# Performance work log

Hardware: AMD Instinct MI355X
Metric: run time of the kernel (lower is better)

Reference implementation:

```python
import jax, jax.numpy as jnp
import numpy as np

N, F, H, C = 4096, 512, 8, 128
LEAKY_ALPHA = 0.2
MASK_VAL = -10e9  # spektral uses -10e9 * (1 - A)


def setup_inputs() -> dict:
    key = jax.random.key(0)
    k1, k2, k3, k4, k5 = jax.random.split(key, 5)
    X = jax.random.normal(k1, (N, F), dtype=jnp.float32)
    # sparse-ish binary adjacency with self loops (dense layout as the layer expects)
    A = (jax.random.uniform(k2, (N, N)) < 0.01).astype(jnp.float32)
    A = jnp.maximum(A, jnp.eye(N, dtype=jnp.float32))
    W = jax.random.normal(k3, (H, F, C), dtype=jnp.float32) * (1.0 / np.sqrt(F))
    a_self = jax.random.normal(k4, (H, C), dtype=jnp.float32) * (1.0 / np.sqrt(C))
    a_neigh = jax.random.normal(k5, (H, C), dtype=jnp.float32) * (1.0 / np.sqrt(C))
    bias = jnp.zeros((H, C), dtype=jnp.float32)
    return {"X": X, "A": A, "W": W, "a_self": a_self, "a_neigh": a_neigh, "bias": bias}


def reference(X, A, W, a_self, a_neigh, bias):
    # per-head feature projection: [H, N, C]
    feats = jnp.einsum("nf,hfc->hnc", X, W)
    # attention scores e_ij = LeakyReLU(a_self . h_i + a_neigh . h_j)
    s_self = jnp.einsum("hnc,hc->hn", feats, a_self)    # [H, N]
    s_neigh = jnp.einsum("hnc,hc->hn", feats, a_neigh)  # [H, N]
    dense = s_self[:, :, None] + s_neigh[:, None, :]    # [H, N, N]
    dense = jnp.where(dense > 0, dense, LEAKY_ALPHA * dense)
    # adjacency mask then row softmax (dropout_rate=0 -> identity)
    dense = dense + MASK_VAL * (1.0 - A)[None, :, :]
    coef = jax.nn.softmax(dense, axis=-1)               # [H, N, N]
    out = jnp.einsum("hnm,hmc->hnc", coef, feats)       # [H, N, C]
    out = out + bias[:, None, :]
    # concat heads: [N, H*C]
    out = jnp.transpose(out, (1, 0, 2)).reshape(N, H * C)
    return jax.nn.relu(out)
```

## Files before the change

### kernel.cpp

```cpp
#include <hip/hip_runtime.h>
#include <hip/hip_bf16.h>

#define GN 4096
#define GF 512
#define GH 8
#define GC 128
#define CAP 256
#define XS 72

typedef __hip_bfloat16 bf16;
typedef unsigned short u16;
typedef unsigned int u32;
typedef __attribute__((ext_vector_type(8))) short bf16x8;
typedef __attribute__((ext_vector_type(4))) float f32x4;

static __device__ inline u16 f2u16(float x) {
    union { bf16 b; u16 u; } cv;
    cv.b = __float2bfloat16(x);
    return cv.u;
}

__global__ __launch_bounds__(256) void prep_csr_kernel(
    const float* __restrict__ A, const float* __restrict__ X,
    const float* __restrict__ W, int* __restrict__ deg,
    u16* __restrict__ lists, u16* __restrict__ Xb, u16* __restrict__ WT)
{
    __shared__ u16 sT[16][520];
    int tid = threadIdx.x;
    int b   = blockIdx.x;

    if (b < 1024) {
        size_t idx = ((size_t)b * 256 + tid) * 8;
        float4 v0 = *(const float4*)(X + idx);
        float4 v1 = *(const float4*)(X + idx + 4);
        u16 o[8] = {f2u16(v0.x), f2u16(v0.y), f2u16(v0.z), f2u16(v0.w),
                    f2u16(v1.x), f2u16(v1.y), f2u16(v1.z), f2u16(v1.w)};
        *(bf16x8*)(Xb + idx) = *(bf16x8*)o;
        return;
    }
    if (b < 1088) {
        int wb = b - 1024;
        int h  = wb >> 3;
        int s16 = (wb & 7) * 16;
        const float* Wh = W + (size_t)h * GF * GC;
        for (int pass = 0; pass < 8; ++pass) {
            int k  = pass * 64 + (tid >> 2);
            int n4 = tid & 3;
            float4 v = *(const float4*)&Wh[(size_t)k * GC + s16 + n4 * 4];
            sT[n4 * 4 + 0][k] = f2u16(v.x);
            sT[n4 * 4 + 1][k] = f2u16(v.y);
            sT[n4 * 4 + 2][k] = f2u16(v.z);
            sT[n4 * 4 + 3][k] = f2u16(v.w);
        }
        __syncthreads();
        int n = tid >> 4, seg = tid & 15;
        u16* dst = WT + ((size_t)h * GC + s16 + n) * GF + seg * 32;
#pragma unroll
        for (int s = 0; s < 4; ++s)
            *(bf16x8*)(dst + s * 8) = *(const bf16x8*)&sT[n][seg * 32 + s * 8];
        return;
    }

    int i    = b - 1088;
    int lane = tid & 63;
    int* cnt = (int*)&sT[0][0];
    if (tid == 0) *cnt = 0;
    __syncthreads();

    u16* row = lists + (size_t)i * CAP;
    const float4* Arow = (const float4*)(A + (size_t)i * GN);
    unsigned long long ltmask = (lane == 63) ? ~0ull >> 1
                                             : (1ull << lane) - 1;
#pragma unroll
    for (int it = 0; it < 4; ++it) {
        int qd = it * 256 + tid;
        float4 a = Arow[qd];
        int j = qd * 4;
#pragma unroll
        for (int comp = 0; comp < 4; ++comp) {
            float av = comp == 0 ? a.x : comp == 1 ? a.y : comp == 2 ? a.z : a.w;
            bool flag = av > 0.5f;
            unsigned long long m = __ballot(flag);
            if (m) {
                int base = 0;
                if (lane == 0) base = atomicAdd(cnt, __popcll(m));
                base = __shfl(base, 0);
                if (flag) {
                    int s = base + __popcll(m & ltmask);
                    if (s < CAP) row[s] = (u16)(j + comp);
                }
            }
        }
    }
    __syncthreads();
    if (tid == 0) deg[i] = *cnt < CAP ? *cnt : CAP;
}

__global__ __launch_bounds__(256) void feats_kernel(
    const u16* __restrict__ Xb, const u16* __restrict__ WT,
    const float* __restrict__ a_self, const float* __restrict__ a_neigh,
    bf16* __restrict__ featsb, float* __restrict__ s_self,
    float* __restrict__ s_neigh)
{
    __shared__ u16 sX[64 * XS];
    __shared__ u16 sW[128 * XS];

    int h   = blockIdx.x >> 6;
    int n0  = (blockIdx.x & 63) << 6;
    int tid = threadIdx.x;
    int lane = tid & 63, wv = tid >> 6;
    int lm = lane & 15, q = lane >> 4;

    const u16* Xp = Xb + (size_t)n0 * GF;
    const u16* Wp = WT + (size_t)h * GC * GF;

    uint4 xr[2], wr[4];

#define ISSUE_TILE(K0)                                                        \
    {                                                                         \
        _Pragma("unroll")                                                     \
        for (int it = 0; it < 2; ++it) {                                      \
            int idx = it * 256 + tid, row = idx >> 3, c = idx & 7;            \
            xr[it] = *(const uint4*)&Xp[(size_t)row * GF + (K0) + c * 8];     \
        }                                                                     \
        _Pragma("unroll")                                                     \
        for (int it = 0; it < 4; ++it) {                                      \
            int idx = it * 256 + tid, row = idx >> 3, c = idx & 7;            \
            wr[it] = *(const uint4*)&Wp[(size_t)row * GF + (K0) + c * 8];     \
        }                                                                     \
    }

#define STORE_TILE()                                                          \
    {                                                                         \
        _Pragma("unroll")                                                     \
        for (int it = 0; it < 2; ++it) {                                      \
            int idx = it * 256 + tid, row = idx >> 3, c = idx & 7;            \
            *(uint4*)&sX[row * XS + c * 8] = xr[it];                          \
        }                                                                     \
        _Pragma("unroll")                                                     \
        for (int it = 0; it < 4; ++it) {                                      \
            int idx = it * 256 + tid, row = idx >> 3, c = idx & 7;            \
            *(uint4*)&sW[row * XS + c * 8] = wr[it];                          \
        }                                                                     \
    }

    f32x4 acc[8];
#pragma unroll
    for (int nt = 0; nt < 8; ++nt) acc[nt] = (f32x4){0.f, 0.f, 0.f, 0.f};

    ISSUE_TILE(0)
    STORE_TILE()

    for (int k0 = 0; k0 < GF; k0 += 64) {
        __syncthreads();
        if (k0 + 64 < GF) ISSUE_TILE(k0 + 64)

#pragma unroll
        for (int ks = 0; ks < 64; ks += 32) {
            bf16x8 af = *(const bf16x8*)&sX[(wv * 16 + lm) * XS + ks + q * 8];
            bf16x8 bfr[8];
#pragma unroll
            for (int nt = 0; nt < 8; ++nt)
                bfr[nt] = *(const bf16x8*)&sW[(nt * 16 + lm) * XS + ks + q * 8];
#pragma unroll
            for (int nt = 0; nt < 8; ++nt)
                acc[nt] = __builtin_amdgcn_mfma_f32_16x16x32_bf16(
                    af, bfr[nt], acc[nt], 0, 0, 0);
        }
        __syncthreads();
        if (k0 + 64 < GF) STORE_TILE()
    }
#undef ISSUE_TILE
#undef STORE_TILE

    float aS[8], aN[8];
#pragma unroll
    for (int nt = 0; nt < 8; ++nt) {
        aS[nt] = a_self[h * GC + nt * 16 + lm];
        aN[nt] = a_neigh[h * GC + nt * 16 + lm];
    }
    float vs[4] = {0.f, 0.f, 0.f, 0.f};
    float vn[4] = {0.f, 0.f, 0.f, 0.f};
    int rbase = n0 + wv * 16 + q * 4;
#pragma unroll
    for (int nt = 0; nt < 8; ++nt) {
        f32x4 v = acc[nt];
        int col = nt * 16 + lm;
#pragma unroll
        for (int r = 0; r < 4; ++r) {
            featsb[((size_t)h * GN + rbase + r) * GC + col] = __float2bfloat16(v[r]);
            vs[r] += v[r] * aS[nt];
            vn[r] += v[r] * aN[nt];
        }
    }
#pragma unroll
    for (int r = 0; r < 4; ++r) {
        for (int off = 1; off < 16; off <<= 1) {
            vs[r] += __shfl_xor(vs[r], off);
            vn[r] += __shfl_xor(vn[r], off);
        }
        if (lm == 0) {
            s_self[h * GN + rbase + r]  = vs[r];
            s_neigh[h * GN + rbase + r] = vn[r];
        }
    }
}

__global__ __launch_bounds__(256) void attn_kernel(
    const int* __restrict__ deg, const u16* __restrict__ lists,
    const float* __restrict__ bias, const bf16* __restrict__ featsb,
    const float* __restrict__ s_self, const float* __restrict__ s_neigh,
    float* __restrict__ out)
{
    int tid  = threadIdx.x;
    int wv   = tid >> 6, lane = tid & 63;
    int g    = blockIdx.x * 4 + wv;
    int h    = g >> 12;
    int i    = g & (GN - 1);

    __shared__ float2 pjbuf[4][CAP];
    float2* pj = pjbuf[wv];

    int M = deg[i];
    const u16* row = lists + (size_t)i * CAP;
    float ssi = s_self[h * GN + i];
    const float* snh = s_neigh + h * GN;

    float lmax = -1e30f;
    for (int k = lane; k < M; k += 64) {
        int j = row[k];
        float e = ssi + snh[j];
        e = e > 0.f ? e : 0.2f * e;
        pj[k] = make_float2(e, __int_as_float(j));
        lmax = fmaxf(lmax, e);
    }
#pragma unroll
    for (int off = 32; off > 0; off >>= 1)
        lmax = fmaxf(lmax, __shfl_xor(lmax, off));

    float lsum = 0.f;
    for (int k = lane; k < M; k += 64) {
        float e = __expf(pj[k].x - lmax);
        pj[k].x = e;
        lsum += e;
    }
#pragma unroll
    for (int off = 32; off > 0; off >>= 1) lsum += __shfl_xor(lsum, off);
    float inv = 1.f / lsum;

    const u32* fh = (const u32*)(featsb + (size_t)h * GN * GC) + lane;
    float acc0 = 0.f, acc1 = 0.f;
#pragma unroll 4
    for (int k = 0; k < M; ++k) {
        float2 v = pj[k];
        int j = __float_as_int(v.y);
        u32 u = fh[(size_t)j << 6];
        acc0 += v.x * __uint_as_float(u << 16);
        acc1 += v.x * __uint_as_float(u & 0xffff0000u);
    }

    const float2 bv = *(const float2*)&bias[h * GC + 2 * lane];
    float r0 = acc0 * inv + bv.x;
    float r1 = acc1 * inv + bv.y;
    float2* op = (float2*)&out[(size_t)i * (GH * GC) + h * GC + 2 * lane];
    *op = make_float2(fmaxf(r0, 0.f), fmaxf(r1, 0.f));
}

extern "C" void kernel_launch(void* const* d_in, const int* in_sizes, int n_in,
                              void* d_out, int out_size, void* d_ws, size_t ws_size,
                              hipStream_t stream)
{
    const float* X       = (const float*)d_in[0];
    const float* A       = (const float*)d_in[1];
    const float* W       = (const float*)d_in[2];
    const float* a_self  = (const float*)d_in[3];
    const float* a_neigh = (const float*)d_in[4];
    const float* bias    = (const float*)d_in[5];
    float* out = (float*)d_out;

    bf16*  featsb  = (bf16*)d_ws;
    float* s_self  = (float*)(featsb + (size_t)GH * GN * GC);
    float* s_neigh = s_self + (size_t)GH * GN;
    int*   deg     = (int*)(s_neigh + (size_t)GH * GN);
    u16*   lists   = (u16*)(deg + GN);
    u16*   Xb      = lists + (size_t)GN * CAP;
    u16*   WT      = Xb + (size_t)GN * GF;

    prep_csr_kernel<<<1088 + GN, 256, 0, stream>>>(A, X, W, deg, lists, Xb, WT);
    feats_kernel<<<GH * 64, 256, 0, stream>>>(Xb, WT, a_self, a_neigh,
                                              featsb, s_self, s_neigh);
    attn_kernel<<<GH * GN / 4, 256, 0, stream>>>(deg, lists, bias, featsb,
                                                 s_self, s_neigh, out);
}
```

Baseline: 178.2 us.

## Process two heads per wavefront in attention kernel to share neighbor lists

Each wavefront in the attention kernel now handles two heads for the same node. The neighbor list, degree and index loads are shared across both heads, and the grid is halved to match. The aggregation loop is unrolled by two with split accumulators so more independent gathers are in flight. The cost is double the LDS per wave (float4 entries) and more registers, which may lower occupancy.

```diff
diff --git a/kernel.cpp b/kernel.cpp
--- a/kernel.cpp
+++ b/kernel.cpp
@@ -215,55 +215,93 @@
     int tid  = threadIdx.x;
     int wv   = tid >> 6, lane = tid & 63;
     int g    = blockIdx.x * 4 + wv;
-    int h    = g >> 12;
+    int hp   = g >> 12;
     int i    = g & (GN - 1);
-
-    __shared__ float2 pjbuf[4][CAP];
-    float2* pj = pjbuf[wv];
+    int h0   = hp * 2, h1 = h0 + 1;
+
+    __shared__ float4 pjbuf[4][CAP];
+    float4* pj = pjbuf[wv];
 
     int M = deg[i];
     const u16* row = lists + (size_t)i * CAP;
-    float ssi = s_self[h * GN + i];
-    const float* snh = s_neigh + h * GN;
-
-    float lmax = -1e30f;
+    float ssi0 = s_self[h0 * GN + i];
+    float ssi1 = s_self[h1 * GN + i];
+    const float* sn0 = s_neigh + (size_t)h0 * GN;
+    const float* sn1 = s_neigh + (size_t)h1 * GN;
+
+    float m0 = -1e30f, m1 = -1e30f;
     for (int k = lane; k < M; k += 64) {
         int j = row[k];
-        float e = ssi + snh[j];
-        e = e > 0.f ? e : 0.2f * e;
-        pj[k] = make_float2(e, __int_as_float(j));
-        lmax = fmaxf(lmax, e);
-    }
-#pragma unroll
-    for (int off = 32; off > 0; off >>= 1)
-        lmax = fmaxf(lmax, __shfl_xor(lmax, off));
-
-    float lsum = 0.f;
+        float e0 = ssi0 + sn0[j]; e0 = e0 > 0.f ? e0 : 0.2f * e0;
+        float e1 = ssi1 + sn1[j]; e1 = e1 > 0.f ? e1 : 0.2f * e1;
+        pj[k] = make_float4(e0, e1, __int_as_float(j), 0.f);
+        m0 = fmaxf(m0, e0);
+        m1 = fmaxf(m1, e1);
+    }
+#pragma unroll
+    for (int off = 32; off > 0; off >>= 1) {
+        m0 = fmaxf(m0, __shfl_xor(m0, off));
+        m1 = fmaxf(m1, __shfl_xor(m1, off));
+    }
+
+    float s0 = 0.f, s1 = 0.f;
     for (int k = lane; k < M; k += 64) {
-        float e = __expf(pj[k].x - lmax);
-        pj[k].x = e;
-        lsum += e;
-    }
-#pragma unroll
-    for (int off = 32; off > 0; off >>= 1) lsum += __shfl_xor(lsum, off);
-    float inv = 1.f / lsum;
-
-    const u32* fh = (const u32*)(featsb + (size_t)h * GN * GC) + lane;
-    float acc0 = 0.f, acc1 = 0.f;
-#pragma unroll 4
-    for (int k = 0; k < M; ++k) {
-        float2 v = pj[k];
-        int j = __float_as_int(v.y);
-        u32 u = fh[(size_t)j << 6];
-        acc0 += v.x * __uint_as_float(u << 16);
-        acc1 += v.x * __uint_as_float(u & 0xffff0000u);
-    }
-
-    const float2 bv = *(const float2*)&bias[h * GC + 2 * lane];
-    float r0 = acc0 * inv + bv.x;
-    float r1 = acc1 * inv + bv.y;
-    float2* op = (float2*)&out[(size_t)i * (GH * GC) + h * GC + 2 * lane];
-    *op = make_float2(fmaxf(r0, 0.f), fmaxf(r1, 0.f));
+        float4 v = pj[k];
+        float e0 = __expf(v.x - m0);
+        float e1 = __expf(v.y - m1);
+        pj[k].x = e0;
+        pj[k].y = e1;
+        s0 += e0;
+        s1 += e1;
+    }
+#pragma unroll
+    for (int off = 32; off > 0; off >>= 1) {
+        s0 += __shfl_xor(s0, off);
+        s1 += __shfl_xor(s1, off);
+    }
+    float inv0 = 1.f / s0, inv1 = 1.f / s1;
+
+    const u32* f0 = (const u32*)(featsb + (size_t)h0 * GN * GC) + lane;
+    const u32* f1 = (const u32*)(featsb + (size_t)h1 * GN * GC) + lane;
+    float aE0 = 0.f, aE1 = 0.f, bE0 = 0.f, bE1 = 0.f;
+    float aO0 = 0.f, aO1 = 0.f, bO0 = 0.f, bO1 = 0.f;
+    int k = 0;
+    for (; k + 2 <= M; k += 2) {
+        float4 v0 = pj[k], v1 = pj[k + 1];
+        int j0 = __float_as_int(v0.z), j1 = __float_as_int(v1.z);
+        u32 u00 = f0[(size_t)j0 << 6];
+        u32 u10 = f1[(size_t)j0 << 6];
+        u32 u01 = f0[(size_t)j1 << 6];
+        u32 u11 = f1[(size_t)j1 << 6];
+        aE0 += v0.x * __uint_as_float(u00 << 16);
+        aE1 += v0.x * __uint_as_float(u00 & 0xffff0000u);
+        bE0 += v0.y * __uint_as_float(u10 << 16);
+        bE1 += v0.y * __uint_as_float(u10 & 0xffff0000u);
+        aO0 += v1.x * __uint_as_float(u01 << 16);
+        aO1 += v1.x * __uint_as_float(u01 & 0xffff0000u);
+        bO0 += v1.y * __uint_as_float(u11 << 16);
+        bO1 += v1.y * __uint_as_float(u11 & 0xffff0000u);
+    }
+    if (k < M) {
+        float4 v0 = pj[k];
+        int j0 = __float_as_int(v0.z);
+        u32 u00 = f0[(size_t)j0 << 6];
+        u32 u10 = f1[(size_t)j0 << 6];
+        aE0 += v0.x * __uint_as_float(u00 << 16);
+        aE1 += v0.x * __uint_as_float(u00 & 0xffff0000u);
+        bE0 += v0.y * __uint_as_float(u10 << 16);
+        bE1 += v0.y * __uint_as_float(u10 & 0xffff0000u);
+    }
+
+    const float2 bv0 = *(const float2*)&bias[h0 * GC + 2 * lane];
+    const float2 bv1 = *(const float2*)&bias[h1 * GC + 2 * lane];
+    size_t ob = (size_t)i * (GH * GC);
+    float2* op0 = (float2*)&out[ob + h0 * GC + 2 * lane];
+    float2* op1 = (float2*)&out[ob + h1 * GC + 2 * lane];
+    *op0 = make_float2(fmaxf((aE0 + aO0) * inv0 + bv0.x, 0.f),
+                       fmaxf((aE1 + aO1) * inv0 + bv0.y, 0.f));
+    *op1 = make_float2(fmaxf((bE0 + bO0) * inv1 + bv1.x, 0.f),
+                       fmaxf((bE1 + bO1) * inv1 + bv1.y, 0.f));
 }
 
 extern "C" void kernel_launch(void* const* d_in, const int* in_sizes, int n_in,
@@ -289,6 +327,6 @@
     prep_csr_kernel<<<1088 + GN, 256, 0, stream>>>(A, X, W, deg, lists, Xb, WT);
     feats_kernel<<<GH * 64, 256, 0, stream>>>(Xb, WT, a_self, a_neigh,
                                               featsb, s_self, s_neigh);
-    attn_kernel<<<GH * GN / 4, 256, 0, stream>>>(deg, lists, bias, featsb,
+    attn_kernel<<<GH * GN / 8, 256, 0, stream>>>(deg, lists, bias, featsb,
                                                  s_self, s_neigh, out);
 }
```

Measured after the change: 171.1 us, median of 2. -4.0%, faster.
